# Kernel optimization log

Measured on AMD Instinct MI355X. Metric: run time of the kernel, lower is better.

Reference implementation:

```python
import jax, jax.numpy as jnp
import numpy as np

N, E, CIN, H, OUT, L = 100000, 1200000, 3, 64, 3, 3
EPS = 1e-7  # GENConv message epsilon


def setup_inputs() -> dict:
    key = jax.random.key(0)
    ks = jax.random.split(key, 8)
    f = lambda k, s, sc=0.1: (jax.random.normal(k, s, jnp.float32) * sc)
    return {
        "x": f(ks[0], (N, CIN), 1.0),
        "edge_index": jax.random.randint(ks[1], (2, E), 0, N, jnp.int32),
        "enc_W": f(ks[2], (CIN, H)),
        "enc_b": jnp.zeros((H,), jnp.float32),
        "t": jnp.ones((L,), jnp.float32),
        "mlp_W1": f(ks[3], (L, H, 2 * H)),
        "mlp_b1": jnp.zeros((L, 2 * H), jnp.float32),
        "mlp_g": jnp.ones((L, 2 * H), jnp.float32),
        "mlp_beta": jnp.zeros((L, 2 * H), jnp.float32),
        "mlp_W2": f(ks[4], (L, 2 * H, H)),
        "mlp_b2": jnp.zeros((L, H), jnp.float32),
        "ln_g": jnp.ones((L, H), jnp.float32),
        "ln_b": jnp.zeros((L, H), jnp.float32),
        "lin_W": f(ks[5], (H, OUT)),
        "lin_b": jnp.zeros((OUT,), jnp.float32),
    }


def layer_norm(x, g, b, eps=1e-5):
    mu = jnp.mean(x, -1, keepdims=True)
    var = jnp.var(x, -1, keepdims=True)
    return (x - mu) * jax.lax.rsqrt(var + eps) * g + b


def genconv(x, src, dst, t, W1, b1, g, beta, W2, b2):
    # message: relu(x_j) + eps, per edge  [E, H]
    msg = jax.nn.relu(x[src]) + EPS
    # softmax aggregation with temperature t (per-destination, elementwise)
    logits = msg * t
    m = jax.ops.segment_max(logits, dst, num_segments=N)            # [N, H]
    w = jnp.exp(logits - m[dst])                                    # [E, H]
    denom = jax.ops.segment_sum(w, dst, num_segments=N)             # [N, H]
    agg = jax.ops.segment_sum(msg * (w / denom[dst]), dst, num_segments=N)
    # root residual + MLP [H -> 2H -> LN -> ReLU -> H]
    out = agg + x
    h = jax.nn.relu(layer_norm(out @ W1 + b1, g, beta))
    return h @ W2 + b2


def reference(x, edge_index, enc_W, enc_b, t, mlp_W1, mlp_b1, mlp_g, mlp_beta,
              mlp_W2, mlp_b2, ln_g, ln_b, lin_W, lin_b):
    src, dst = edge_index[0], edge_index[1]
    h = x @ enc_W + enc_b
    # layers[0].conv applied directly (DeepGCN 'res+' convention)
    h = genconv(h, src, dst, t[0], mlp_W1[0], mlp_b1[0], mlp_g[0], mlp_beta[0],
                mlp_W2[0], mlp_b2[0])
    for i in range(1, L):
        z = jax.nn.relu(layer_norm(h, ln_g[i], ln_b[i]))
        h = h + genconv(z, src, dst, t[i], mlp_W1[i], mlp_b1[i], mlp_g[i],
                        mlp_beta[i], mlp_W2[i], mlp_b2[i])
    h = jax.nn.relu(layer_norm(h, ln_g[0], ln_b[0]))
    return h @ lin_W + lin_b
```

## Files before the change

### kernel.cpp

```cpp
#include <hip/hip_runtime.h>
#include <hip/hip_bf16.h>
#include <math.h>

#define H 64
#define H2 128
#define EPS_MSG 1e-7f
#define LN_EPS 1e-5f
#define LOG2E 1.4426950408889634f
#define LN2 0.6931471805599453f
#define YSTR 136
#define BUCK_CAP 5120
#define CHUNK 8192
#define PADSLACK 768

typedef __attribute__((ext_vector_type(8))) short bf16x8;
typedef __attribute__((ext_vector_type(4))) float f32x4;

__device__ __forceinline__ unsigned short f2bf(float f) {
    union { float f; unsigned int i; } x; x.f = f;
    unsigned int r = x.i + 0x7FFF + ((x.i >> 16) & 1);
    return (unsigned short)(r >> 16);
}

__global__ __launch_bounds__(256) void bhist_k(const int* __restrict__ dst,
                                               int* __restrict__ bsize, int E, int nbuck) {
    __shared__ int h[512];
    for (int i = threadIdx.x; i < nbuck; i += 256) h[i] = 0;
    __syncthreads();
    int lo = blockIdx.x * CHUNK;
    int hi = lo + CHUNK; if (hi > E) hi = E;
    for (int i = lo + threadIdx.x; i < hi; i += 256)
        atomicAdd(&h[dst[i] >> 8], 1);
    __syncthreads();
    for (int i = threadIdx.x; i < nbuck; i += 256)
        if (h[i]) atomicAdd(&bsize[i], h[i]);
}

__global__ __launch_bounds__(512) void bscan_k(const int* __restrict__ bsize,
                                               int* __restrict__ bstart, int* __restrict__ bcursor,
                                               int nbuck, int E) {
    __shared__ int tmp[512];
    int tid = threadIdx.x;
    int v = (tid < nbuck) ? bsize[tid] : 0;
    tmp[tid] = v;
    __syncthreads();
    #pragma unroll
    for (int off = 1; off < 512; off <<= 1) {
        int t = (tid >= off) ? tmp[tid - off] : 0;
        __syncthreads();
        tmp[tid] += t;
        __syncthreads();
    }
    if (tid < nbuck) {
        int excl = tmp[tid] - v;
        bstart[tid] = excl;
        bcursor[tid] = excl;
    }
    if (tid == 0) bstart[nbuck] = E;
}

__global__ __launch_bounds__(256) void bscat_k(const int* __restrict__ src,
                                               const int* __restrict__ dst,
                                               int* __restrict__ bcursor,
                                               unsigned int* __restrict__ bdata,
                                               int E, int nbuck) {
    __shared__ int h[512], base[512];
    for (int i = threadIdx.x; i < nbuck; i += 256) h[i] = 0;
    __syncthreads();
    int lo = blockIdx.x * CHUNK;
    int hi = lo + CHUNK; if (hi > E) hi = E;
    for (int i = lo + threadIdx.x; i < hi; i += 256)
        atomicAdd(&h[dst[i] >> 8], 1);
    __syncthreads();
    for (int i = threadIdx.x; i < nbuck; i += 256) {
        int c = h[i];
        base[i] = c ? atomicAdd(&bcursor[i], c) : 0;
        h[i] = 0;
    }
    __syncthreads();
    for (int i = lo + threadIdx.x; i < hi; i += 256) {
        int d = dst[i];
        int b = d >> 8;
        int pos = base[b] + atomicAdd(&h[b], 1);
        bdata[pos] = ((unsigned int)src[i] << 8) | (unsigned int)(d & 255);
    }
}

__global__ __launch_bounds__(256) void bsort_k(const unsigned int* __restrict__ bdata,
                                               const int* __restrict__ bstart,
                                               int* __restrict__ row_beg, int* __restrict__ row_end,
                                               int* __restrict__ srcs_sorted,
                                               int Nn) {
    __shared__ unsigned int stage[BUCK_CAP];
    __shared__ int cnt[256], pre[256], ex[256];
    int b = blockIdx.x, tid = threadIdx.x;
    int lo = bstart[b], hi = bstart[b + 1];
    int m = hi - lo; if (m > BUCK_CAP) m = BUCK_CAP;
    int pLo = lo + b * PADSLACK;
    for (int i = tid; i < m; i += 256) stage[i] = bdata[lo + i];
    cnt[tid] = 0;
    __syncthreads();
    for (int i = tid; i < m; i += 256) atomicAdd(&cnt[stage[i] & 255], 1);
    __syncthreads();
    int myc = cnt[tid];
    int pc = (myc + 3) & ~3;
    pre[tid] = pc;
    __syncthreads();
    #pragma unroll
    for (int off = 1; off < 256; off <<= 1) {
        int t = (tid >= off) ? pre[tid - off] : 0;
        __syncthreads();
        pre[tid] += t;
        __syncthreads();
    }
    int pexcl = pre[tid] - pc;
    ex[tid] = pexcl;
    int node = (b << 8) + tid;
    if (node < Nn) {
        row_beg[node] = pLo + pexcl;
        row_end[node] = pLo + pexcl + pc;
    }
    for (int p = myc; p < pc; ++p) srcs_sorted[pLo + pexcl + p] = Nn;
    __syncthreads();
    cnt[tid] = 0;
    __syncthreads();
    for (int i = tid; i < m; i += 256) {
        unsigned int v = stage[i];
        int dl = v & 255;
        int p = ex[dl] + atomicAdd(&cnt[dl], 1);
        srcs_sorted[pLo + p] = (int)(v >> 8);
    }
}

__global__ void wprep_k(const float* __restrict__ W1, const float* __restrict__ W2,
                        unsigned short* __restrict__ Wf1, unsigned short* __restrict__ Wf2) {
    int idx = blockIdx.x * 256 + threadIdx.x;
    const int half = 3 * 8192;
    if (idx < half) {
        int layer = idx / 8192, rem = idx - layer * 8192;
        int t = rem >> 9;
        int l = (rem >> 3) & 63;
        int i = rem & 7;
        int h = t >> 3, ct = t & 7;
        int kpos = h * 32 + (l >> 4) * 8 + i;
        int k = (kpos & 3) * 16 + (kpos >> 2);
        int j = ct * 16 + (l & 15);
        Wf1[idx] = f2bf(W1[(size_t)layer * H * H2 + (size_t)k * H2 + j]);
    } else if (idx < 2 * half) {
        int id2 = idx - half;
        int layer = id2 / 8192, rem = id2 - layer * 8192;
        int t = rem >> 9;
        int l = (rem >> 3) & 63;
        int i = rem & 7;
        int kk = t >> 2, ct2 = t & 3;
        int k = kk * 32 + (l >> 4) * 8 + i;
        int j = ct2 * 16 + (l & 15);
        Wf2[id2] = f2bf(W2[(size_t)layer * H2 * H + (size_t)k * H + j]);
    }
}

__global__ void encoder_k(const float* __restrict__ x, const float* __restrict__ W,
                          const float* __restrict__ b,
                          unsigned short* __restrict__ Zself, unsigned short* __restrict__ Zmsg,
                          const float* __restrict__ t, int Nn) {
    int idx = blockIdx.x * blockDim.x + threadIdx.x;
    if (idx >= (Nn + 1) * H) return;
    int n = idx >> 6, c = idx & 63;
    if (n == Nn) { Zmsg[idx] = f2bf(-200.f); return; }
    float acc = b[c];
    #pragma unroll
    for (int k = 0; k < 3; ++k) acc = fmaf(x[n * 3 + k], W[k * H + c], acc);
    int j = (c & 15) * 4 + (c >> 4);
    Zself[(size_t)n * H + j] = f2bf(acc);
    Zmsg[(size_t)n * H + j]  = f2bf(fmaxf(acc, 0.f) * (LOG2E) * t[0]);
}

__global__ __launch_bounds__(256) void gather_k(
    const unsigned short* __restrict__ Zmsg, const unsigned short* __restrict__ Zself,
    unsigned short* __restrict__ Gbf,
    const int* __restrict__ row_beg, const int* __restrict__ row_end,
    const int* __restrict__ srcs,
    const float* __restrict__ t, int layer, int Nn)
{
    int wid = threadIdx.x >> 6, lane = threadIdx.x & 63;
    int n = blockIdx.x * 4 + wid;
    if (n >= Nn) return;
    int beg = row_beg[n];
    int nIter = (row_end[n] - beg) >> 2;
    const int* sp = srcs + beg;
    int slot = lane >> 4;
    int ch4  = lane & 15;

    float ds0 = 0.f, ds1 = 0.f, ds2 = 0.f, ds3 = 0.f;
    float ss0 = 0.f, ss1 = 0.f, ss2 = 0.f, ss3 = 0.f;

    #define LQ(qq, i)                                                          \
        {                                                                      \
            int s = sp[4 * (i) + slot];                                        \
            qq = *(const uint2*)(Zmsg + (size_t)s * H + ch4 * 4);              \
        }

    #define PROCF(qq)                                                          \
        {                                                                      \
            float u0 = __uint_as_float(qq.x << 16);                            \
            float u1 = __uint_as_float(qq.x & 0xffff0000u);                    \
            float u2 = __uint_as_float(qq.y << 16);                            \
            float u3 = __uint_as_float(qq.y & 0xffff0000u);                    \
            float w0 = __builtin_amdgcn_exp2f(u0);                             \
            float w1 = __builtin_amdgcn_exp2f(u1);                             \
            float w2 = __builtin_amdgcn_exp2f(u2);                             \
            float w3 = __builtin_amdgcn_exp2f(u3);                             \
            ds0 += w0; ds1 += w1; ds2 += w2; ds3 += w3;                        \
            ss0 = fmaf(u0, w0, ss0); ss1 = fmaf(u1, w1, ss1);                  \
            ss2 = fmaf(u2, w2, ss2); ss3 = fmaf(u3, w3, ss3);                  \
        }

    if (nIter > 0) {
        uint2 q0 = {0,0}, q1 = {0,0}, q2 = {0,0}, q3 = {0,0};
        LQ(q0, 0)
        if (nIter > 1) LQ(q1, 1)
        if (nIter > 2) LQ(q2, 2)
        if (nIter > 3) LQ(q3, 3)
        int i = 0;
        #pragma unroll 1
        for (; i + 4 < nIter; i += 4) {
            PROCF(q0) LQ(q0, i + 4)
            PROCF(q1) if (i + 5 < nIter) LQ(q1, i + 5)
            PROCF(q2) if (i + 6 < nIter) LQ(q2, i + 6)
            PROCF(q3) if (i + 7 < nIter) LQ(q3, i + 7)
        }
        PROCF(q0)
        if (i + 1 < nIter) PROCF(q1)
        if (i + 2 < nIter) PROCF(q2)
        if (i + 3 < nIter) PROCF(q3)
    }
    #undef LQ
    #undef PROCF

    #pragma unroll
    for (int o = 16; o <= 32; o <<= 1) {
        ds0 += __shfl_xor(ds0, o, 64); ds1 += __shfl_xor(ds1, o, 64);
        ds2 += __shfl_xor(ds2, o, 64); ds3 += __shfl_xor(ds3, o, 64);
        ss0 += __shfl_xor(ss0, o, 64); ss1 += __shfl_xor(ss1, o, 64);
        ss2 += __shfl_xor(ss2, o, 64); ss3 += __shfl_xor(ss3, o, 64);
    }

    if (slot == 0) {
        float scale = (LN2) * __builtin_amdgcn_rcpf(t[layer]);
        uint2 sv = *(const uint2*)(Zself + (size_t)n * H + ch4 * 4);
        float o0 = __uint_as_float(sv.x << 16);
        float o1 = __uint_as_float(sv.x & 0xffff0000u);
        float o2 = __uint_as_float(sv.y << 16);
        float o3 = __uint_as_float(sv.y & 0xffff0000u);
        if (nIter > 0) {
            o0 += fmaf(ss0 * __builtin_amdgcn_rcpf(ds0), scale, EPS_MSG);
            o1 += fmaf(ss1 * __builtin_amdgcn_rcpf(ds1), scale, EPS_MSG);
            o2 += fmaf(ss2 * __builtin_amdgcn_rcpf(ds2), scale, EPS_MSG);
            o3 += fmaf(ss3 * __builtin_amdgcn_rcpf(ds3), scale, EPS_MSG);
        }
        uint2 pv;
        pv.x = (unsigned int)f2bf(o0) | ((unsigned int)f2bf(o1) << 16);
        pv.y = (unsigned int)f2bf(o2) | ((unsigned int)f2bf(o3) << 16);
        *(uint2*)(Gbf + (size_t)n * H + ch4 * 4) = pv;
    }
}

__global__ __launch_bounds__(256) void mlp_k(
    const unsigned short* __restrict__ Gbf, float* __restrict__ B,
    const unsigned short* __restrict__ Wf1, const unsigned short* __restrict__ Wf2,
    const float* __restrict__ b1, const float* __restrict__ g,
    const float* __restrict__ beta, const float* __restrict__ b2,
    unsigned short* __restrict__ Zself, unsigned short* __restrict__ Zmsg,
    const float* __restrict__ tptr, const float* __restrict__ ln_g,
    const float* __restrict__ ln_b, const float* __restrict__ lin_W,
    const float* __restrict__ lin_b, float* __restrict__ outp,
    int wlayer, int lnidx, int resid, int mode, int Nn)
{
    __shared__ __align__(16) unsigned short yt[4][16 * YSTR];
    int wid = threadIdx.x >> 6, lane = threadIdx.x & 63;
    int gq = lane >> 4, c = lane & 15;
    int n0 = (blockIdx.x * 4 + wid) * 16;

    Wf1 += (size_t)wlayer * 8192; Wf2 += (size_t)wlayer * 8192;
    b1 += wlayer * H2; g += wlayer * H2; beta += wlayer * H2; b2 += wlayer * H;

    int nA = n0 + c; if (nA >= Nn) nA = Nn - 1;
    bf16x8 a0 = *(const bf16x8*)(Gbf + (size_t)nA * H + gq * 8);
    bf16x8 a1 = *(const bf16x8*)(Gbf + (size_t)nA * H + 32 + gq * 8);

    f32x4 acc[8];
    #pragma unroll
    for (int ct = 0; ct < 8; ++ct) {
        f32x4 z = {0.f, 0.f, 0.f, 0.f};
        bf16x8 w0 = *(const bf16x8*)(Wf1 + (size_t)(ct * 64 + lane) * 8);
        bf16x8 w1 = *(const bf16x8*)(Wf1 + (size_t)((8 + ct) * 64 + lane) * 8);
        z = __builtin_amdgcn_mfma_f32_16x16x32_bf16(a0, w0, z, 0, 0, 0);
        z = __builtin_amdgcn_mfma_f32_16x16x32_bf16(a1, w1, z, 0, 0, 0);
        acc[ct] = z;
    }

    float v[8][4];
    #pragma unroll
    for (int ct = 0; ct < 8; ++ct) {
        float bias = b1[ct * 16 + c];
        #pragma unroll
        for (int r = 0; r < 4; ++r) v[ct][r] = acc[ct][r] + bias;
    }
    float mean[4], inv[4];
    #pragma unroll
    for (int r = 0; r < 4; ++r) {
        float s = 0.f;
        #pragma unroll
        for (int ct = 0; ct < 8; ++ct) s += v[ct][r];
        #pragma unroll
        for (int o = 1; o < 16; o <<= 1) s += __shfl_xor(s, o, 64);
        mean[r] = s * (1.f / H2);
    }
    #pragma unroll
    for (int r = 0; r < 4; ++r) {
        float s = 0.f;
        #pragma unroll
        for (int ct = 0; ct < 8; ++ct) { float d = v[ct][r] - mean[r]; s = fmaf(d, d, s); }
        #pragma unroll
        for (int o = 1; o < 16; o <<= 1) s += __shfl_xor(s, o, 64);
        inv[r] = rsqrtf(s * (1.f / H2) + LN_EPS);
    }
    unsigned short* Y = yt[wid];
    #pragma unroll
    for (int ct = 0; ct < 8; ++ct) {
        float gg = g[ct * 16 + c], bb = beta[ct * 16 + c];
        #pragma unroll
        for (int r = 0; r < 4; ++r) {
            float yv = fmaxf(fmaf((v[ct][r] - mean[r]) * inv[r], gg, bb), 0.f);
            Y[(gq * 4 + r) * YSTR + ct * 16 + c] = f2bf(yv);
        }
    }

    f32x4 acc2[4];
    #pragma unroll
    for (int t = 0; t < 4; ++t) acc2[t] = (f32x4){0.f, 0.f, 0.f, 0.f};
    #pragma unroll
    for (int kk = 0; kk < 4; ++kk) {
        bf16x8 af = *(const bf16x8*)(Y + c * YSTR + kk * 32 + gq * 8);
        #pragma unroll
        for (int t = 0; t < 4; ++t) {
            bf16x8 wf = *(const bf16x8*)(Wf2 + (size_t)((kk * 4 + t) * 64 + lane) * 8);
            acc2[t] = __builtin_amdgcn_mfma_f32_16x16x32_bf16(af, wf, acc2[t], 0, 0, 0);
        }
    }

    float b2v[4], gg2[4], bb2[4], lw[4][3];
    const float* g64 = ln_g + lnidx * H;
    const float* be64 = ln_b + lnidx * H;
    #pragma unroll
    for (int tt = 0; tt < 4; ++tt) {
        b2v[tt] = b2[tt * 16 + c];
        gg2[tt] = g64[tt * 16 + c];
        bb2[tt] = be64[tt * 16 + c];
    }
    if (mode == 1) {
        #pragma unroll
        for (int tt = 0; tt < 4; ++tt)
            #pragma unroll
            for (int k = 0; k < 3; ++k) lw[tt][k] = lin_W[(tt * 16 + c) * 3 + k];
    }
    float kmsg = (mode == 0) ? (LOG2E * tptr[lnidx]) : 0.f;

    #pragma unroll
    for (int r = 0; r < 4; ++r) {
        int n = n0 + gq * 4 + r;
        int nc = (n < Nn) ? n : (Nn - 1);
        float hv[4];
        #pragma unroll
        for (int tt = 0; tt < 4; ++tt) hv[tt] = acc2[tt][r] + b2v[tt];
        if (resid) {
            float4 old = *(const float4*)&B[(size_t)nc * H + c * 4];
            hv[0] += old.x; hv[1] += old.y; hv[2] += old.z; hv[3] += old.w;
        }
        float s = hv[0] + hv[1] + hv[2] + hv[3];
        #pragma unroll
        for (int o = 1; o < 16; o <<= 1) s += __shfl_xor(s, o, 64);
        float mu = s * (1.f / H);
        float q = 0.f;
        #pragma unroll
        for (int tt = 0; tt < 4; ++tt) { float d = hv[tt] - mu; q = fmaf(d, d, q); }
        #pragma unroll
        for (int o = 1; o < 16; o <<= 1) q += __shfl_xor(q, o, 64);
        float iv = rsqrtf(q * (1.f / H) + LN_EPS);
        float z[4];
        #pragma unroll
        for (int tt = 0; tt < 4; ++tt)
            z[tt] = fmaxf(fmaf((hv[tt] - mu) * iv, gg2[tt], bb2[tt]), 0.f);

        if (mode == 0) {
            if (n < Nn) {
                float4 hq = {hv[0], hv[1], hv[2], hv[3]};
                *(float4*)&B[(size_t)n * H + c * 4] = hq;
                uint2 zs;
                zs.x = (unsigned int)f2bf(z[0]) | ((unsigned int)f2bf(z[1]) << 16);
                zs.y = (unsigned int)f2bf(z[2]) | ((unsigned int)f2bf(z[3]) << 16);
                *(uint2*)&Zself[(size_t)n * H + c * 4] = zs;
                uint2 zm;
                zm.x = (unsigned int)f2bf(z[0] * kmsg) | ((unsigned int)f2bf(z[1] * kmsg) << 16);
                zm.y = (unsigned int)f2bf(z[2] * kmsg) | ((unsigned int)f2bf(z[3] * kmsg) << 16);
                *(uint2*)&Zmsg[(size_t)n * H + c * 4] = zm;
            }
        } else {
            float p0 = 0.f, p1 = 0.f, p2 = 0.f;
            #pragma unroll
            for (int tt = 0; tt < 4; ++tt) {
                p0 = fmaf(z[tt], lw[tt][0], p0);
                p1 = fmaf(z[tt], lw[tt][1], p1);
                p2 = fmaf(z[tt], lw[tt][2], p2);
            }
            #pragma unroll
            for (int o = 1; o < 16; o <<= 1) {
                p0 += __shfl_xor(p0, o, 64);
                p1 += __shfl_xor(p1, o, 64);
                p2 += __shfl_xor(p2, o, 64);
            }
            if (c == 0 && n < Nn) {
                outp[(size_t)n * 3 + 0] = p0 + lin_b[0];
                outp[(size_t)n * 3 + 1] = p1 + lin_b[1];
                outp[(size_t)n * 3 + 2] = p2 + lin_b[2];
            }
        }
    }
}

extern "C" void kernel_launch(void* const* d_in, const int* in_sizes, int n_in,
                              void* d_out, int out_size, void* d_ws, size_t ws_size,
                              hipStream_t stream) {
    const float* x        = (const float*)d_in[0];
    const int*   eidx     = (const int*)  d_in[1];
    const float* enc_W    = (const float*)d_in[2];
    const float* enc_b    = (const float*)d_in[3];
    const float* t        = (const float*)d_in[4];
    const float* mlp_W1   = (const float*)d_in[5];
    const float* mlp_b1   = (const float*)d_in[6];
    const float* mlp_g    = (const float*)d_in[7];
    const float* mlp_beta = (const float*)d_in[8];
    const float* mlp_W2   = (const float*)d_in[9];
    const float* mlp_b2   = (const float*)d_in[10];
    const float* ln_g     = (const float*)d_in[11];
    const float* ln_b     = (const float*)d_in[12];
    const float* lin_W    = (const float*)d_in[13];
    const float* lin_b    = (const float*)d_in[14];
    float* out = (float*)d_out;

    const int N = in_sizes[0] / 3;
    const int E = in_sizes[1] / 2;
    const int* src = eidx;
    const int* dst = eidx + E;
    const int nbuck = (N + 255) >> 8;

    float* Bm = (float*)d_ws;
    int* row_beg   = (int*)(Bm + (size_t)N * H);
    int* row_end   = row_beg + N;
    int* bsize     = row_end + N;
    int* bstart    = bsize + 512;
    int* bcursor   = bstart + 513;
    int* srcs_sorted = bcursor + 512;
    unsigned short* Zself = (unsigned short*)(srcs_sorted + E + 512 * PADSLACK);
    unsigned short* Zmsg  = Zself + (size_t)N * H;
    unsigned short* Gbf   = Zmsg + (size_t)(N + 1) * H;
    unsigned short* Wf1   = Gbf + (size_t)N * H;
    unsigned short* Wf2   = Wf1 + 3 * 8192;
    unsigned int* bdata = (unsigned int*)Gbf;

    const int eBlocks = (E + CHUNK - 1) / CHUNK;

    hipMemsetAsync(bsize, 0, 512 * sizeof(int), stream);
    bhist_k<<<eBlocks, 256, 0, stream>>>(dst, bsize, E, nbuck);
    bscan_k<<<1, 512, 0, stream>>>(bsize, bstart, bcursor, nbuck, E);
    bscat_k<<<eBlocks, 256, 0, stream>>>(src, dst, bcursor, bdata, E, nbuck);
    bsort_k<<<nbuck, 256, 0, stream>>>(bdata, bstart, row_beg, row_end, srcs_sorted, N);

    wprep_k<<<192, 256, 0, stream>>>(mlp_W1, mlp_W2, Wf1, Wf2);
    encoder_k<<<((size_t)(N + 1) * H + 255) / 256, 256, 0, stream>>>(x, enc_W, enc_b, Zself, Zmsg, t, N);

    const int blocks4   = (N + 3) / 4;
    const int mlpBlocks = (N + 63) / 64;

    gather_k<<<blocks4, 256, 0, stream>>>(Zmsg, Zself, Gbf, row_beg, row_end, srcs_sorted, t, 0, N);
    mlp_k<<<mlpBlocks, 256, 0, stream>>>(Gbf, Bm, Wf1, Wf2, mlp_b1, mlp_g, mlp_beta, mlp_b2,
                                         Zself, Zmsg, t, ln_g, ln_b, lin_W, lin_b, out,
                                         0, 1, 0, 0, N);
    gather_k<<<blocks4, 256, 0, stream>>>(Zmsg, Zself, Gbf, row_beg, row_end, srcs_sorted, t, 1, N);
    mlp_k<<<mlpBlocks, 256, 0, stream>>>(Gbf, Bm, Wf1, Wf2, mlp_b1, mlp_g, mlp_beta, mlp_b2,
                                         Zself, Zmsg, t, ln_g, ln_b, lin_W, lin_b, out,
                                         1, 2, 1, 0, N);
    gather_k<<<blocks4, 256, 0, stream>>>(Zmsg, Zself, Gbf, row_beg, row_end, srcs_sorted, t, 2, N);
    mlp_k<<<mlpBlocks, 256, 0, stream>>>(Gbf, Bm, Wf1, Wf2, mlp_b1, mlp_g, mlp_beta, mlp_b2,
                                         Zself, Zmsg, t, ln_g, ln_b, lin_W, lin_b, out,
                                         2, 0, 1, 1, N);
}
```

Before: 375.8 us.

## Use fixed-stride buckets, gather two nodes per wave, drop Zself writes

Edge bucketing now writes into fixed-stride per-bucket slots, which removes the separate histogram and scan kernels and one pass over dst. The gather kernel handles two destination nodes per wavefront with interleaved loads to raise memory-level parallelism. For layers after the first it rebuilds the self term from Zmsg by rescaling, so the MLP no longer writes Zself. The fixed bucket capacity silently drops edges if any bucket exceeds BSTRIDE, and rebuilding the self value from the scaled bf16 copy adds a little rounding.

New measurement: 339.7 us. 9.6% less time.

```diff
diff --git a/kernel.cpp b/kernel.cpp
--- a/kernel.cpp
+++ b/kernel.cpp
@@ -9,9 +9,9 @@
 #define LOG2E 1.4426950408889634f
 #define LN2 0.6931471805599453f
 #define YSTR 136
-#define BUCK_CAP 5120
+#define BSTRIDE 4608
+#define OSTRIDE 5376
 #define CHUNK 8192
-#define PADSLACK 768
 
 typedef __attribute__((ext_vector_type(8))) short bf16x8;
 typedef __attribute__((ext_vector_type(4))) float f32x4;
@@ -22,9 +22,12 @@
     return (unsigned short)(r >> 16);
 }
 
-__global__ __launch_bounds__(256) void bhist_k(const int* __restrict__ dst,
-                                               int* __restrict__ bsize, int E, int nbuck) {
-    __shared__ int h[512];
+__global__ __launch_bounds__(256) void bscat_k(const int* __restrict__ src,
+                                               const int* __restrict__ dst,
+                                               int* __restrict__ bcnt,
+                                               unsigned int* __restrict__ bdata,
+                                               int E, int nbuck) {
+    __shared__ int h[512], base[512];
     for (int i = threadIdx.x; i < nbuck; i += 256) h[i] = 0;
     __syncthreads();
     int lo = blockIdx.x * CHUNK;
@@ -32,49 +35,9 @@
     for (int i = lo + threadIdx.x; i < hi; i += 256)
         atomicAdd(&h[dst[i] >> 8], 1);
     __syncthreads();
-    for (int i = threadIdx.x; i < nbuck; i += 256)
-        if (h[i]) atomicAdd(&bsize[i], h[i]);
-}
-
-__global__ __launch_bounds__(512) void bscan_k(const int* __restrict__ bsize,
-                                               int* __restrict__ bstart, int* __restrict__ bcursor,
-                                               int nbuck, int E) {
-    __shared__ int tmp[512];
-    int tid = threadIdx.x;
-    int v = (tid < nbuck) ? bsize[tid] : 0;
-    tmp[tid] = v;
-    __syncthreads();
-    #pragma unroll
-    for (int off = 1; off < 512; off <<= 1) {
-        int t = (tid >= off) ? tmp[tid - off] : 0;
-        __syncthreads();
-        tmp[tid] += t;
-        __syncthreads();
-    }
-    if (tid < nbuck) {
-        int excl = tmp[tid] - v;
-        bstart[tid] = excl;
-        bcursor[tid] = excl;
-    }
-    if (tid == 0) bstart[nbuck] = E;
-}
-
-__global__ __launch_bounds__(256) void bscat_k(const int* __restrict__ src,
-                                               const int* __restrict__ dst,
-                                               int* __restrict__ bcursor,
-                                               unsigned int* __restrict__ bdata,
-                                               int E, int nbuck) {
-    __shared__ int h[512], base[512];
-    for (int i = threadIdx.x; i < nbuck; i += 256) h[i] = 0;
-    __syncthreads();
-    int lo = blockIdx.x * CHUNK;
-    int hi = lo + CHUNK; if (hi > E) hi = E;
-    for (int i = lo + threadIdx.x; i < hi; i += 256)
-        atomicAdd(&h[dst[i] >> 8], 1);
-    __syncthreads();
     for (int i = threadIdx.x; i < nbuck; i += 256) {
         int c = h[i];
-        base[i] = c ? atomicAdd(&bcursor[i], c) : 0;
+        base[i] = c ? atomicAdd(&bcnt[i], c) : 0;
         h[i] = 0;
     }
     __syncthreads();
@@ -82,21 +45,21 @@
         int d = dst[i];
         int b = d >> 8;
         int pos = base[b] + atomicAdd(&h[b], 1);
-        bdata[pos] = ((unsigned int)src[i] << 8) | (unsigned int)(d & 255);
+        bdata[(size_t)b * BSTRIDE + pos] = ((unsigned int)src[i] << 8) | (unsigned int)(d & 255);
     }
 }
 
 __global__ __launch_bounds__(256) void bsort_k(const unsigned int* __restrict__ bdata,
-                                               const int* __restrict__ bstart,
+                                               const int* __restrict__ bcnt,
                                                int* __restrict__ row_beg, int* __restrict__ row_end,
                                                int* __restrict__ srcs_sorted,
                                                int Nn) {
-    __shared__ unsigned int stage[BUCK_CAP];
+    __shared__ unsigned int stage[BSTRIDE];
     __shared__ int cnt[256], pre[256], ex[256];
     int b = blockIdx.x, tid = threadIdx.x;
-    int lo = bstart[b], hi = bstart[b + 1];
-    int m = hi - lo; if (m > BUCK_CAP) m = BUCK_CAP;
-    int pLo = lo + b * PADSLACK;
+    int m = bcnt[b]; if (m > BSTRIDE) m = BSTRIDE;
+    size_t lo = (size_t)b * BSTRIDE;
+    int oLo = b * OSTRIDE;
     for (int i = tid; i < m; i += 256) stage[i] = bdata[lo + i];
     cnt[tid] = 0;
     __syncthreads();
@@ -117,10 +80,10 @@
     ex[tid] = pexcl;
     int node = (b << 8) + tid;
     if (node < Nn) {
-        row_beg[node] = pLo + pexcl;
-        row_end[node] = pLo + pexcl + pc;
-    }
-    for (int p = myc; p < pc; ++p) srcs_sorted[pLo + pexcl + p] = Nn;
+        row_beg[node] = oLo + pexcl;
+        row_end[node] = oLo + pexcl + pc;
+    }
+    for (int p = myc; p < pc; ++p) srcs_sorted[oLo + pexcl + p] = Nn;
     __syncthreads();
     cnt[tid] = 0;
     __syncthreads();
@@ -128,7 +91,7 @@
         unsigned int v = stage[i];
         int dl = v & 255;
         int p = ex[dl] + atomicAdd(&cnt[dl], 1);
-        srcs_sorted[pLo + p] = (int)(v >> 8);
+        srcs_sorted[oLo + p] = (int)(v >> 8);
     }
 }
 
@@ -183,24 +146,32 @@
     const float* __restrict__ t, int layer, int Nn)
 {
     int wid = threadIdx.x >> 6, lane = threadIdx.x & 63;
-    int n = blockIdx.x * 4 + wid;
-    if (n >= Nn) return;
-    int beg = row_beg[n];
-    int nIter = (row_end[n] - beg) >> 2;
-    const int* sp = srcs + beg;
+    int nA = blockIdx.x * 8 + wid * 2;
+    if (nA >= Nn) return;
+    int nB = nA + 1;
+    bool hasB = (nB < Nn);
     int slot = lane >> 4;
     int ch4  = lane & 15;
-
-    float ds0 = 0.f, ds1 = 0.f, ds2 = 0.f, ds3 = 0.f;
-    float ss0 = 0.f, ss1 = 0.f, ss2 = 0.f, ss3 = 0.f;
-
-    #define LQ(qq, i)                                                          \
+    float scale = (LN2) * __builtin_amdgcn_rcpf(t[layer]);
+
+    int begA = row_beg[nA];
+    int itA  = (row_end[nA] - begA) >> 2;
+    int begB = hasB ? row_beg[nB] : begA;
+    int itB  = hasB ? (row_end[nB] - begB) >> 2 : 0;
+    const int* spA = srcs + begA;
+    const int* spB = srcs + begB;
+
+    const unsigned short* selfTab = (layer == 0) ? Zself : Zmsg;
+    uint2 svA = *(const uint2*)(selfTab + (size_t)nA * H + ch4 * 4);
+    uint2 svB = hasB ? *(const uint2*)(selfTab + (size_t)nB * H + ch4 * 4) : svA;
+
+    #define LQ(qq, sp, i)                                                      \
         {                                                                      \
             int s = sp[4 * (i) + slot];                                        \
             qq = *(const uint2*)(Zmsg + (size_t)s * H + ch4 * 4);              \
         }
 
-    #define PROCF(qq)                                                          \
+    #define PROC(qq, d0, d1, d2, d3, s0, s1, s2, s3)                           \
         {                                                                      \
             float u0 = __uint_as_float(qq.x << 16);                            \
             float u1 = __uint_as_float(qq.x & 0xffff0000u);                    \
@@ -210,58 +181,107 @@
             float w1 = __builtin_amdgcn_exp2f(u1);                             \
             float w2 = __builtin_amdgcn_exp2f(u2);                             \
             float w3 = __builtin_amdgcn_exp2f(u3);                             \
-            ds0 += w0; ds1 += w1; ds2 += w2; ds3 += w3;                        \
-            ss0 = fmaf(u0, w0, ss0); ss1 = fmaf(u1, w1, ss1);                  \
-            ss2 = fmaf(u2, w2, ss2); ss3 = fmaf(u3, w3, ss3);                  \
-        }
-
-    if (nIter > 0) {
-        uint2 q0 = {0,0}, q1 = {0,0}, q2 = {0,0}, q3 = {0,0};
-        LQ(q0, 0)
-        if (nIter > 1) LQ(q1, 1)
-        if (nIter > 2) LQ(q2, 2)
-        if (nIter > 3) LQ(q3, 3)
+            d0 += w0; d1 += w1; d2 += w2; d3 += w3;                            \
+            s0 = fmaf(u0, w0, s0); s1 = fmaf(u1, w1, s1);                      \
+            s2 = fmaf(u2, w2, s2); s3 = fmaf(u3, w3, s3);                      \
+        }
+    #define PROCA(qq) PROC(qq, dA0, dA1, dA2, dA3, sA0, sA1, sA2, sA3)
+    #define PROCB(qq) PROC(qq, dB0, dB1, dB2, dB3, sB0, sB1, sB2, sB3)
+
+    uint2 a0 = {0,0}, a1 = {0,0}, a2 = {0,0}, a3 = {0,0};
+    uint2 b0 = {0,0}, b1 = {0,0}, b2 = {0,0}, b3 = {0,0};
+    if (itA > 0) LQ(a0, spA, 0)
+    if (itB > 0) LQ(b0, spB, 0)
+    if (itA > 1) LQ(a1, spA, 1)
+    if (itB > 1) LQ(b1, spB, 1)
+    if (itA > 2) LQ(a2, spA, 2)
+    if (itB > 2) LQ(b2, spB, 2)
+    if (itA > 3) LQ(a3, spA, 3)
+    if (itB > 3) LQ(b3, spB, 3)
+
+    float dA0=0.f,dA1=0.f,dA2=0.f,dA3=0.f,sA0=0.f,sA1=0.f,sA2=0.f,sA3=0.f;
+    float dB0=0.f,dB1=0.f,dB2=0.f,dB3=0.f,sB0=0.f,sB1=0.f,sB2=0.f,sB3=0.f;
+
+    if (itA > 0) {
         int i = 0;
         #pragma unroll 1
-        for (; i + 4 < nIter; i += 4) {
-            PROCF(q0) LQ(q0, i + 4)
-            PROCF(q1) if (i + 5 < nIter) LQ(q1, i + 5)
-            PROCF(q2) if (i + 6 < nIter) LQ(q2, i + 6)
-            PROCF(q3) if (i + 7 < nIter) LQ(q3, i + 7)
-        }
-        PROCF(q0)
-        if (i + 1 < nIter) PROCF(q1)
-        if (i + 2 < nIter) PROCF(q2)
-        if (i + 3 < nIter) PROCF(q3)
+        for (; i + 4 < itA; i += 4) {
+            PROCA(a0) LQ(a0, spA, i + 4)
+            PROCA(a1) if (i + 5 < itA) LQ(a1, spA, i + 5)
+            PROCA(a2) if (i + 6 < itA) LQ(a2, spA, i + 6)
+            PROCA(a3) if (i + 7 < itA) LQ(a3, spA, i + 7)
+        }
+        PROCA(a0)
+        if (i + 1 < itA) PROCA(a1)
+        if (i + 2 < itA) PROCA(a2)
+        if (i + 3 < itA) PROCA(a3)
+    }
+    if (itB > 0) {
+        int i = 0;
+        #pragma unroll 1
+        for (; i + 4 < itB; i += 4) {
+            PROCB(b0) LQ(b0, spB, i + 4)
+            PROCB(b1) if (i + 5 < itB) LQ(b1, spB, i + 5)
+            PROCB(b2) if (i + 6 < itB) LQ(b2, spB, i + 6)
+            PROCB(b3) if (i + 7 < itB) LQ(b3, spB, i + 7)
+        }
+        PROCB(b0)
+        if (i + 1 < itB) PROCB(b1)
+        if (i + 2 < itB) PROCB(b2)
+        if (i + 3 < itB) PROCB(b3)
     }
     #undef LQ
-    #undef PROCF
+    #undef PROC
+    #undef PROCA
+    #undef PROCB
 
     #pragma unroll
     for (int o = 16; o <= 32; o <<= 1) {
-        ds0 += __shfl_xor(ds0, o, 64); ds1 += __shfl_xor(ds1, o, 64);
-        ds2 += __shfl_xor(ds2, o, 64); ds3 += __shfl_xor(ds3, o, 64);
-        ss0 += __shfl_xor(ss0, o, 64); ss1 += __shfl_xor(ss1, o, 64);
-        ss2 += __shfl_xor(ss2, o, 64); ss3 += __shfl_xor(ss3, o, 64);
+        dA0 += __shfl_xor(dA0, o, 64); dA1 += __shfl_xor(dA1, o, 64);
+        dA2 += __shfl_xor(dA2, o, 64); dA3 += __shfl_xor(dA3, o, 64);
+        sA0 += __shfl_xor(sA0, o, 64); sA1 += __shfl_xor(sA1, o, 64);
+        sA2 += __shfl_xor(sA2, o, 64); sA3 += __shfl_xor(sA3, o, 64);
+        dB0 += __shfl_xor(dB0, o, 64); dB1 += __shfl_xor(dB1, o, 64);
+        dB2 += __shfl_xor(dB2, o, 64); dB3 += __shfl_xor(dB3, o, 64);
+        sB0 += __shfl_xor(sB0, o, 64); sB1 += __shfl_xor(sB1, o, 64);
+        sB2 += __shfl_xor(sB2, o, 64); sB3 += __shfl_xor(sB3, o, 64);
     }
 
     if (slot == 0) {
-        float scale = (LN2) * __builtin_amdgcn_rcpf(t[layer]);
-        uint2 sv = *(const uint2*)(Zself + (size_t)n * H + ch4 * 4);
-        float o0 = __uint_as_float(sv.x << 16);
-        float o1 = __uint_as_float(sv.x & 0xffff0000u);
-        float o2 = __uint_as_float(sv.y << 16);
-        float o3 = __uint_as_float(sv.y & 0xffff0000u);
-        if (nIter > 0) {
-            o0 += fmaf(ss0 * __builtin_amdgcn_rcpf(ds0), scale, EPS_MSG);
-            o1 += fmaf(ss1 * __builtin_amdgcn_rcpf(ds1), scale, EPS_MSG);
-            o2 += fmaf(ss2 * __builtin_amdgcn_rcpf(ds2), scale, EPS_MSG);
-            o3 += fmaf(ss3 * __builtin_amdgcn_rcpf(ds3), scale, EPS_MSG);
-        }
-        uint2 pv;
-        pv.x = (unsigned int)f2bf(o0) | ((unsigned int)f2bf(o1) << 16);
-        pv.y = (unsigned int)f2bf(o2) | ((unsigned int)f2bf(o3) << 16);
-        *(uint2*)(Gbf + (size_t)n * H + ch4 * 4) = pv;
+        {
+            float o0 = __uint_as_float(svA.x << 16);
+            float o1 = __uint_as_float(svA.x & 0xffff0000u);
+            float o2 = __uint_as_float(svA.y << 16);
+            float o3 = __uint_as_float(svA.y & 0xffff0000u);
+            if (layer != 0) { o0 *= scale; o1 *= scale; o2 *= scale; o3 *= scale; }
+            if (itA > 0) {
+                o0 += fmaf(sA0 * __builtin_amdgcn_rcpf(dA0), scale, EPS_MSG);
+                o1 += fmaf(sA1 * __builtin_amdgcn_rcpf(dA1), scale, EPS_MSG);
+                o2 += fmaf(sA2 * __builtin_amdgcn_rcpf(dA2), scale, EPS_MSG);
+                o3 += fmaf(sA3 * __builtin_amdgcn_rcpf(dA3), scale, EPS_MSG);
+            }
+            uint2 pv;
+            pv.x = (unsigned int)f2bf(o0) | ((unsigned int)f2bf(o1) << 16);
+            pv.y = (unsigned int)f2bf(o2) | ((unsigned int)f2bf(o3) << 16);
+            *(uint2*)(Gbf + (size_t)nA * H + ch4 * 4) = pv;
+        }
+        if (hasB) {
+            float o0 = __uint_as_float(svB.x << 16);
+            float o1 = __uint_as_float(svB.x & 0xffff0000u);
+            float o2 = __uint_as_float(svB.y << 16);
+            float o3 = __uint_as_float(svB.y & 0xffff0000u);
+            if (layer != 0) { o0 *= scale; o1 *= scale; o2 *= scale; o3 *= scale; }
+            if (itB > 0) {
+                o0 += fmaf(sB0 * __builtin_amdgcn_rcpf(dB0), scale, EPS_MSG);
+                o1 += fmaf(sB1 * __builtin_amdgcn_rcpf(dB1), scale, EPS_MSG);
+                o2 += fmaf(sB2 * __builtin_amdgcn_rcpf(dB2), scale, EPS_MSG);
+                o3 += fmaf(sB3 * __builtin_amdgcn_rcpf(dB3), scale, EPS_MSG);
+            }
+            uint2 pv;
+            pv.x = (unsigned int)f2bf(o0) | ((unsigned int)f2bf(o1) << 16);
+            pv.y = (unsigned int)f2bf(o2) | ((unsigned int)f2bf(o3) << 16);
+            *(uint2*)(Gbf + (size_t)nB * H + ch4 * 4) = pv;
+        }
     }
 }
 
@@ -270,7 +290,7 @@
     const unsigned short* __restrict__ Wf1, const unsigned short* __restrict__ Wf2,
     const float* __restrict__ b1, const float* __restrict__ g,
     const float* __restrict__ beta, const float* __restrict__ b2,
-    unsigned short* __restrict__ Zself, unsigned short* __restrict__ Zmsg,
+    unsigned short* __restrict__ Zmsg,
     const float* __restrict__ tptr, const float* __restrict__ ln_g,
     const float* __restrict__ ln_b, const float* __restrict__ lin_W,
     const float* __restrict__ lin_b, float* __restrict__ outp,
@@ -396,10 +416,6 @@
             if (n < Nn) {
                 float4 hq = {hv[0], hv[1], hv[2], hv[3]};
                 *(float4*)&B[(size_t)n * H + c * 4] = hq;
-                uint2 zs;
-                zs.x = (unsigned int)f2bf(z[0]) | ((unsigned int)f2bf(z[1]) << 16);
-                zs.y = (unsigned int)f2bf(z[2]) | ((unsigned int)f2bf(z[3]) << 16);
-                *(uint2*)&Zself[(size_t)n * H + c * 4] = zs;
                 uint2 zm;
                 zm.x = (unsigned int)f2bf(z[0] * kmsg) | ((unsigned int)f2bf(z[1] * kmsg) << 16);
                 zm.y = (unsigned int)f2bf(z[2] * kmsg) | ((unsigned int)f2bf(z[3] * kmsg) << 16);
@@ -457,11 +473,9 @@
     float* Bm = (float*)d_ws;
     int* row_beg   = (int*)(Bm + (size_t)N * H);
     int* row_end   = row_beg + N;
-    int* bsize     = row_end + N;
-    int* bstart    = bsize + 512;
-    int* bcursor   = bstart + 513;
-    int* srcs_sorted = bcursor + 512;
-    unsigned short* Zself = (unsigned short*)(srcs_sorted + E + 512 * PADSLACK);
+    int* bcnt      = row_end + N;
+    int* srcs_sorted = bcnt + 512;
+    unsigned short* Zself = (unsigned short*)(srcs_sorted + 512 * OSTRIDE);
     unsigned short* Zmsg  = Zself + (size_t)N * H;
     unsigned short* Gbf   = Zmsg + (size_t)(N + 1) * H;
     unsigned short* Wf1   = Gbf + (size_t)N * H;
@@ -470,28 +484,26 @@
 
     const int eBlocks = (E + CHUNK - 1) / CHUNK;
 
-    hipMemsetAsync(bsize, 0, 512 * sizeof(int), stream);
-    bhist_k<<<eBlocks, 256, 0, stream>>>(dst, bsize, E, nbuck);
-    bscan_k<<<1, 512, 0, stream>>>(bsize, bstart, bcursor, nbuck, E);
-    bscat_k<<<eBlocks, 256, 0, stream>>>(src, dst, bcursor, bdata, E, nbuck);
-    bsort_k<<<nbuck, 256, 0, stream>>>(bdata, bstart, row_beg, row_end, srcs_sorted, N);
+    hipMemsetAsync(bcnt, 0, 512 * sizeof(int), stream);
+    bscat_k<<<eBlocks, 256, 0, stream>>>(src, dst, bcnt, bdata, E, nbuck);
+    bsort_k<<<nbuck, 256, 0, stream>>>(bdata, bcnt, row_beg, row_end, srcs_sorted, N);
 
     wprep_k<<<192, 256, 0, stream>>>(mlp_W1, mlp_W2, Wf1, Wf2);
     encoder_k<<<((size_t)(N + 1) * H + 255) / 256, 256, 0, stream>>>(x, enc_W, enc_b, Zself, Zmsg, t, N);
 
-    const int blocks4   = (N + 3) / 4;
+    const int gBlocks   = (N + 7) / 8;
     const int mlpBlocks = (N + 63) / 64;
 
-    gather_k<<<blocks4, 256, 0, stream>>>(Zmsg, Zself, Gbf, row_beg, row_end, srcs_sorted, t, 0, N);
+    gather_k<<<gBlocks, 256, 0, stream>>>(Zmsg, Zself, Gbf, row_beg, row_end, srcs_sorted, t, 0, N);
     mlp_k<<<mlpBlocks, 256, 0, stream>>>(Gbf, Bm, Wf1, Wf2, mlp_b1, mlp_g, mlp_beta, mlp_b2,
-                                         Zself, Zmsg, t, ln_g, ln_b, lin_W, lin_b, out,
+                                         Zmsg, t, ln_g, ln_b, lin_W, lin_b, out,
                                          0, 1, 0, 0, N);
-    gather_k<<<blocks4, 256, 0, stream>>>(Zmsg, Zself, Gbf, row_beg, row_end, srcs_sorted, t, 1, N);
+    gather_k<<<gBlocks, 256, 0, stream>>>(Zmsg, Zself, Gbf, row_beg, row_end, srcs_sorted, t, 1, N);
     mlp_k<<<mlpBlocks, 256, 0, stream>>>(Gbf, Bm, Wf1, Wf2, mlp_b1, mlp_g, mlp_beta, mlp_b2,
-                                         Zself, Zmsg, t, ln_g, ln_b, lin_W, lin_b, out,
+                                         Zmsg, t, ln_g, ln_b, lin_W, lin_b, out,
                                          1, 2, 1, 0, N);
-    gather_k<<<blocks4, 256, 0, stream>>>(Zmsg, Zself, Gbf, row_beg, row_end, srcs_sorted, t, 2, N);
+    gather_k<<<gBlocks, 256, 0, stream>>>(Zmsg, Zself, Gbf, row_beg, row_end, srcs_sorted, t, 2, N);
     mlp_k<<<mlpBlocks, 256, 0, stream>>>(Gbf, Bm, Wf1, Wf2, mlp_b1, mlp_g, mlp_beta, mlp_b2,
-                                         Zself, Zmsg, t, ln_g, ln_b, lin_W, lin_b, out,
+                                         Zmsg, t, ln_g, ln_b, lin_W, lin_b, out,
                                          2, 0, 1, 1, N);
 }
```
